# Kernel tuning notes

Hardware: AMD Instinct MI355X
Metric: run time of the kernel (lower is better)

The kernel has to match this reference:

```python
import jax, jax.numpy as jnp
import numpy as np

BETA = 0.02  # soft-argmax temperature (CATs / matchsplat default)


def _resize_bilinear_ac(x, out_h, out_w):
    """Bilinear resize over the last two dims, align_corners=True (matches F.interpolate)."""
    H, W = x.shape[-2], x.shape[-1]
    ys = jnp.linspace(0.0, H - 1.0, out_h)
    xs = jnp.linspace(0.0, W - 1.0, out_w)
    y0 = jnp.floor(ys).astype(jnp.int32)
    y1 = jnp.minimum(y0 + 1, H - 1)
    x0 = jnp.floor(xs).astype(jnp.int32)
    x1 = jnp.minimum(x0 + 1, W - 1)
    wy = (ys - y0).astype(x.dtype)
    wx = (xs - x0).astype(x.dtype)
    rows = x[..., y0, :] * (1.0 - wy)[:, None] + x[..., y1, :] * wy[:, None]
    return rows[..., x0] * (1.0 - wx) + rows[..., x1] * wx


def _correlation(f0, f1):
    # f0, f1: [B, C, H, W] -> dense 4D cost volume [B, H0, W0, H1, W1], scaled by 1/sqrt(C)
    b, c, h, w = f0.shape
    return jnp.einsum('bchw,bcuv->bhwuv', f0, f1) / (c ** 0.5)


def _interpolate4d(x, size):
    # x: [B, ch, h1, w1, h2, w2]; separable bilinear over (h2,w2) then (h1,w1), align_corners=True
    B, ch, h1, w1, h2, w2 = x.shape
    x = _resize_bilinear_ac(x.reshape(B, ch * h1 * w1, h2, w2), size[2], size[3])
    x = x.reshape(B, ch, h1, w1, size[2], size[3])
    x = jnp.transpose(x, (0, 1, 4, 5, 2, 3)).reshape(B, ch * size[2] * size[3], h1, w1)
    x = _resize_bilinear_ac(x, size[0], size[1])
    x = x.reshape(B, ch, size[2], size[3], size[0], size[1])
    return jnp.transpose(x, (0, 1, 4, 5, 2, 3))


def _soft_argmax(corr):
    # corr: [B, Hs*Ws, Ht, Wt]; softmax over source positions per target pixel,
    # then marginal expectations of normalized [-1,1] coordinates.
    b, c, h, w = corr.shape
    prob = jax.nn.softmax(corr / BETA, axis=1).reshape(b, h, w, h, w)
    x_normal = jnp.linspace(-1.0, 1.0, w, dtype=corr.dtype)
    y_normal = jnp.linspace(-1.0, 1.0, h, dtype=corr.dtype)
    grid_x = (prob.sum(axis=1) * x_normal[None, :, None, None]).sum(axis=1)[:, None]  # [B,1,h,w]
    grid_y = (prob.sum(axis=2) * y_normal[None, :, None, None]).sum(axis=1)[:, None]
    return grid_x, grid_y


def _mapping_to_flow(mapping):
    # mapping: [B,2,H,W] normalized coords in [-1,1] -> pixel-space flow (map - identity grid)
    B, _, H, W = mapping.shape
    mx = (mapping[:, 0] + 1.0) * (W - 1) / 2.0
    my = (mapping[:, 1] + 1.0) * (H - 1) / 2.0
    gx = jnp.arange(W, dtype=mapping.dtype)[None, :]
    gy = jnp.arange(H, dtype=mapping.dtype)[:, None]
    return jnp.stack([mx - gx, my - gy], axis=1)


def _forward(feat0_c, feat1_c, feat0_f, feat1_f):
    B = feat0_c.shape[0]
    S = 64
    corr_c = _correlation(feat0_c, feat1_c)                        # [B,32,32,32,32]
    corr_c = _interpolate4d(corr_c[:, None], (S, S, S, S))[:, 0]   # [B,64,64,64,64]
    corr_f = _correlation(feat0_f, feat1_f)                        # [B,64,64,64,64]
    c = ((corr_c + corr_f) * 0.5)[:, None]                         # [B,1,64,64,64,64]
    c_flip = jnp.transpose(c, (0, 1, 4, 5, 2, 3))
    gx, gy = _soft_argmax(c_flip.reshape(B, S * S, S, S))
    flow = _mapping_to_flow(jnp.concatenate([gx, gy], axis=1))
    gxf, gyf = _soft_argmax(c.reshape(B, S * S, S, S))
    flow_flip = _mapping_to_flow(jnp.concatenate([gxf, gyf], axis=1))
    trans_features = jnp.stack([feat0_f, feat1_f], axis=1)         # [B,2,C,64,64]
    tc = jnp.stack([feat0_c, feat1_c], axis=1)
    C = tc.shape[2]
    tc = _resize_bilinear_ac(tc.reshape(B * 2, C, tc.shape[-2], tc.shape[-1]), S, S)
    trans_features_coarse = tc.reshape(B, 2, C, S, S)
    return trans_features, trans_features_coarse, c, c_flip, flow, flow_flip


def setup_inputs():
    key = jax.random.key(0)
    k0, k1, k2, k3 = jax.random.split(key, 4)
    B, C = 2, 128
    return {
        'feat0_c': jax.random.normal(k0, (B, C, 32, 32), dtype=jnp.float32),
        'feat1_c': jax.random.normal(k1, (B, C, 32, 32), dtype=jnp.float32),
        'feat0_f': jax.random.normal(k2, (B, C, 64, 64), dtype=jnp.float32),
        'feat1_f': jax.random.normal(k3, (B, C, 64, 64), dtype=jnp.float32),
    }


def reference(feat0_c, feat1_c, feat0_f, feat1_f):
    return _forward(feat0_c, feat1_c, feat0_f, feat1_f)
```

## Files before the change

### kernel.cpp

```cpp
#include <hip/hip_runtime.h>
#include <math.h>

#define SCALE_C 0.08838834764831845f
#define INV_BETA 50.0f
#define STEP63 (2.0f / 63.0f)

typedef short bf16x8 __attribute__((ext_vector_type(8)));
typedef float f32x4 __attribute__((ext_vector_type(4)));

__device__ __forceinline__ void interp_coef32(int t, int& i0, int& i1, float& w) {
    float s = (float)(t * 31) / 63.0f;
    i0 = (int)floorf(s);
    if (i0 > 31) i0 = 31;
    i1 = i0 + 1;
    if (i1 > 31) i1 = 31;
    w = s - (float)i0;
}

__global__ __launch_bounds__(256) void k_corr_c(const float* __restrict__ f0c,
                                                const float* __restrict__ f1c,
                                                float* __restrict__ ws) {
    __shared__ float As[16][64];
    __shared__ float Bs[16][64];
    const int b = blockIdx.z;
    const int m0 = blockIdx.y * 64, n0 = blockIdx.x * 64;
    const float* A  = f0c + (long long)b * 131072;
    const float* Bp = f1c + (long long)b * 131072;
    const int tid = threadIdx.x;
    const int tx = tid & 15, ty = tid >> 4;
    const int lk = tid >> 4;
    const int lc = (tid & 15) * 4;
    float acc[4][4] = {{0.f}};
    for (int k0 = 0; k0 < 128; k0 += 16) {
        *(float4*)&As[lk][lc] = *(const float4*)&A[(k0 + lk) * 1024 + m0 + lc];
        *(float4*)&Bs[lk][lc] = *(const float4*)&Bp[(k0 + lk) * 1024 + n0 + lc];
        __syncthreads();
#pragma unroll
        for (int kk = 0; kk < 16; ++kk) {
            float4 a4 = *(float4*)&As[kk][ty * 4];
            float4 b4 = *(float4*)&Bs[kk][tx * 4];
            float av[4] = {a4.x, a4.y, a4.z, a4.w};
            float bv[4] = {b4.x, b4.y, b4.z, b4.w};
#pragma unroll
            for (int i = 0; i < 4; ++i)
#pragma unroll
                for (int j = 0; j < 4; ++j)
                    acc[i][j] = fmaf(av[i], bv[j], acc[i][j]);
        }
        __syncthreads();
    }
#pragma unroll
    for (int i = 0; i < 4; ++i) {
        float4 w4 = make_float4(acc[i][0] * SCALE_C, acc[i][1] * SCALE_C,
                                acc[i][2] * SCALE_C, acc[i][3] * SCALE_C);
        *(float4*)&ws[(long long)b * 1048576 + (long long)(m0 + ty * 4 + i) * 1024 + n0 + tx * 4] = w4;
    }
}

__global__ __launch_bounds__(256) void k_split(const float* __restrict__ f0f,
                                               const float* __restrict__ f1f,
                                               unsigned short* __restrict__ hi,
                                               unsigned short* __restrict__ lo) {
    __shared__ unsigned int t[64 * 132];
    const int m = blockIdx.y;
    const int pt = blockIdx.x;
    const float* src = ((m >> 1) ? f1f : f0f) + (size_t)(m & 1) * 524288 + pt * 64;
    const int tid = threadIdx.x;
#pragma unroll
    for (int p = 0; p < 8; ++p) {
        int k = p * 16 + (tid >> 4);
        int px = (tid & 15) * 4;
        float4 v = *(const float4*)&src[(size_t)k * 4096 + px];
        float vv[4] = {v.x, v.y, v.z, v.w};
#pragma unroll
        for (int j = 0; j < 4; ++j) {
            float x = vv[j];
            unsigned int u = __float_as_uint(x);
            unsigned int h = (u + 0x7FFFu + ((u >> 16) & 1u)) >> 16;
            float r = x - __uint_as_float(h << 16);
            unsigned int ur = __float_as_uint(r);
            unsigned int l2 = (ur + 0x7FFFu + ((ur >> 16) & 1u)) >> 16;
            t[(px + j) * 132 + k] = h | (l2 << 16);
        }
    }
    __syncthreads();
    const int row = tid >> 2, ks = (tid & 3) * 32;
    size_t obase = ((size_t)m * 4096 + (size_t)pt * 64 + row) * 128 + ks;
#pragma unroll
    for (int c = 0; c < 4; ++c) {
        unsigned int u[8];
        *(uint4*)&u[0] = *(const uint4*)&t[row * 132 + ks + c * 8];
        *(uint4*)&u[4] = *(const uint4*)&t[row * 132 + ks + c * 8 + 4];
        uint4 ho, lw;
        ho.x = (u[0] & 0xFFFFu) | (u[1] << 16);
        ho.y = (u[2] & 0xFFFFu) | (u[3] << 16);
        ho.z = (u[4] & 0xFFFFu) | (u[5] << 16);
        ho.w = (u[6] & 0xFFFFu) | (u[7] << 16);
        lw.x = (u[0] >> 16) | (u[1] & 0xFFFF0000u);
        lw.y = (u[2] >> 16) | (u[3] & 0xFFFF0000u);
        lw.z = (u[4] >> 16) | (u[5] & 0xFFFF0000u);
        lw.w = (u[6] >> 16) | (u[7] & 0xFFFF0000u);
        *(uint4*)&hi[obase + c * 8] = ho;
        *(uint4*)&lo[obase + c * 8] = lw;
    }
}

__global__ __launch_bounds__(256, 3) void k_fused2(const unsigned short* __restrict__ planes,
                                                   const float* __restrict__ cws,
                                                   float* __restrict__ c_out,
                                                   float* __restrict__ cf_out,
                                                   float* __restrict__ parts) {
    __shared__ __attribute__((aligned(16))) float smem[8448];
    const int b = blockIdx.z, by = blockIdx.y, bx = blockIdx.x;
    const int tid = threadIdx.x;
    const int wv = tid >> 6, lane = tid & 63;
    const int lr = lane & 15, lq = lane >> 4;
    const int wr = wv >> 1, wc = wv & 1;

    {
        const float* Cc = cws + (size_t)b * 1048576;
        for (int e = tid; e < 8192; e += 256) {
            int pair = e >> 11, rem = e & 2047;
            int xc0 = rem >> 6, x1 = rem & 63;
            int s0 = pair >> 1, s1 = pair & 1;
            int ya, yb; float wy0; interp_coef32(2 * by + s0, ya, yb, wy0);
            int za, zb; float wy1; interp_coef32(2 * bx + s1, za, zb, wy1);
            int xa, xb; float wx1; interp_coef32(x1, xa, xb, wx1);
            const float* r0 = Cc + (size_t)(ya * 32 + xc0) * 1024;
            const float* r1 = Cc + (size_t)(yb * 32 + xc0) * 1024;
            float g0 = (r0[za * 32 + xa] * (1.f - wy1) + r0[zb * 32 + xa] * wy1) * (1.f - wy0)
                     + (r1[za * 32 + xa] * (1.f - wy1) + r1[zb * 32 + xa] * wy1) * wy0;
            float g1 = (r0[za * 32 + xb] * (1.f - wy1) + r0[zb * 32 + xb] * wy1) * (1.f - wy0)
                     + (r1[za * 32 + xb] * (1.f - wy1) + r1[zb * 32 + xb] * wy1) * wy0;
            smem[(pair * 64 + x1) * 33 + xc0] = g0 * (1.f - wx1) + g1 * wx1;
        }
    }

    const unsigned short* Ah = planes + (size_t)b * 524288       + (size_t)(by * 128 + wr * 64) * 128;
    const unsigned short* Bh = planes + (size_t)(2 + b) * 524288 + (size_t)(bx * 128 + wc * 64) * 128;
    f32x4 acc[4][4];
#pragma unroll
    for (int i = 0; i < 4; ++i)
#pragma unroll
        for (int j = 0; j < 4; ++j) acc[i][j] = (f32x4){0.f, 0.f, 0.f, 0.f};

#pragma unroll 2
    for (int kc = 0; kc < 4; ++kc) {
        const int ko = kc * 32 + lq * 8;
        bf16x8 ah[4], al[4], bh[4], bl[4];
#pragma unroll
        for (int t = 0; t < 4; ++t) {
            const unsigned short* pa = Ah + (size_t)(t * 16 + lr) * 128 + ko;
            const unsigned short* pb = Bh + (size_t)(t * 16 + lr) * 128 + ko;
            ah[t] = *(const bf16x8*)pa;
            al[t] = *(const bf16x8*)(pa + 2097152);
            bh[t] = *(const bf16x8*)pb;
            bl[t] = *(const bf16x8*)(pb + 2097152);
        }
#pragma unroll
        for (int ni = 0; ni < 4; ++ni)
#pragma unroll
            for (int mi = 0; mi < 4; ++mi) {
                f32x4 a = acc[mi][ni];
                a = __builtin_amdgcn_mfma_f32_16x16x32_bf16(ah[mi], bh[ni], a, 0, 0, 0);
                a = __builtin_amdgcn_mfma_f32_16x16x32_bf16(al[mi], bh[ni], a, 0, 0, 0);
                a = __builtin_amdgcn_mfma_f32_16x16x32_bf16(ah[mi], bl[ni], a, 0, 0, 0);
                acc[mi][ni] = a;
            }
    }

    __syncthreads();

#pragma unroll
    for (int mi = 0; mi < 4; ++mi)
#pragma unroll
        for (int dr = 0; dr < 4; ++dr) {
            int x0 = mi * 16 + lq * 4 + dr;
            float s = (float)(x0 * 31) / 63.0f;
            int i0 = (int)s;
            float w = s - (float)i0;
            int i1 = i0 + 1; if (i1 > 31) i1 = 31;
#pragma unroll
            for (int ni = 0; ni < 4; ++ni) {
                const float* t2 = &smem[(wv * 64 + ni * 16 + lr) * 33];
                float up = t2[i0] * (1.f - w) + t2[i1] * w;
                acc[mi][ni][dr] = (acc[mi][ni][dr] * SCALE_C + up) * 0.5f;
            }
        }

    const int rowbase = by * 128 + wr * 64, colbase = bx * 128 + wc * 64;
    {
        size_t fb = ((size_t)b << 24) + (size_t)colbase * 4096 + rowbase;
#pragma unroll
        for (int mi = 0; mi < 4; ++mi)
#pragma unroll
            for (int ni = 0; ni < 4; ++ni) {
                int co = ni * 16 + lr;
                *(float4*)&cf_out[fb + (size_t)co * 4096 + mi * 16 + lq * 4] =
                    make_float4(acc[mi][ni][0], acc[mi][ni][1], acc[mi][ni][2], acc[mi][ni][3]);
            }
    }

#pragma unroll
    for (int r = 0; r < 2; ++r) {
        __syncthreads();
        if (wr == r) {
#pragma unroll
            for (int mi = 0; mi < 4; ++mi)
#pragma unroll
                for (int dr = 0; dr < 4; ++dr) {
                    int rl = mi * 16 + lq * 4 + dr;
                    int sw = (rl & 7) << 2;
#pragma unroll
                    for (int ni = 0; ni < 4; ++ni) {
                        int col = wc * 64 + ni * 16 + lr;
                        int c4 = col >> 2;
                        smem[rl * 132 + ((c4 ^ sw) << 2) + (col & 3)] = acc[mi][ni][dr];
                    }
                }
        }
        __syncthreads();
        size_t cb = ((size_t)b << 24) + (size_t)(by * 128 + r * 64) * 4096 + bx * 128;
#pragma unroll
        for (int i = 0; i < 8; ++i) {
            int f = tid + i * 256;
            int rl = f >> 5, c4 = f & 31;
            float4 v = *(float4*)&smem[rl * 132 + ((c4 ^ ((rl & 7) << 2)) << 2)];
            *(float4*)&c_out[cb + (size_t)rl * 4096 + c4 * 4] = v;
        }
    }

    float4* pred4 = (float4*)smem;
    float4* parts4 = (float4*)parts;
    __syncthreads();

    {
        float yn1 = -1.f + (float)(2 * bx + wc) * STEP63;
#pragma unroll
        for (int mi = 0; mi < 4; ++mi)
#pragma unroll
            for (int dr = 0; dr < 4; ++dr) {
                float m = fmaxf(fmaxf(acc[mi][0][dr], acc[mi][1][dr]),
                                fmaxf(acc[mi][2][dr], acc[mi][3][dr]));
                m = fmaxf(m, __shfl_xor(m, 1, 64));
                m = fmaxf(m, __shfl_xor(m, 2, 64));
                m = fmaxf(m, __shfl_xor(m, 4, 64));
                m = fmaxf(m, __shfl_xor(m, 8, 64));
                float l = 0.f, sx = 0.f;
#pragma unroll
                for (int ni = 0; ni < 4; ++ni) {
                    float e = __expf((acc[mi][ni][dr] - m) * INV_BETA);
                    l += e;
                    sx += e * (-1.f + (float)(ni * 16 + lr) * STEP63);
                }
                l += __shfl_xor(l, 1, 64);  sx += __shfl_xor(sx, 1, 64);
                l += __shfl_xor(l, 2, 64);  sx += __shfl_xor(sx, 2, 64);
                l += __shfl_xor(l, 4, 64);  sx += __shfl_xor(sx, 4, 64);
                l += __shfl_xor(l, 8, 64);  sx += __shfl_xor(sx, 8, 64);
                if (lr == 0)
                    pred4[wc * 128 + wr * 64 + mi * 16 + lq * 4 + dr] = make_float4(m, l, sx, yn1 * l);
            }
    }
    __syncthreads();
    if (tid < 128) {
        float4 h0 = pred4[tid], h1 = pred4[128 + tid];
        float M = fmaxf(h0.x, h1.x);
        float s0 = __expf((h0.x - M) * INV_BETA);
        float s1 = __expf((h1.x - M) * INV_BETA);
        parts4[((size_t)b * 4096 + by * 128 + tid) * 32 + bx] =
            make_float4(M, h0.y * s0 + h1.y * s1, h0.z * s0 + h1.z * s1, h0.w * s0 + h1.w * s1);
    }
    __syncthreads();

    {
        float yn0 = -1.f + (float)(2 * by + wr) * STEP63;
#pragma unroll
        for (int ni = 0; ni < 4; ++ni) {
            float m = acc[0][ni][0];
#pragma unroll
            for (int mi = 0; mi < 4; ++mi)
#pragma unroll
                for (int dr = 0; dr < 4; ++dr) m = fmaxf(m, acc[mi][ni][dr]);
            m = fmaxf(m, __shfl_xor(m, 16, 64));
            m = fmaxf(m, __shfl_xor(m, 32, 64));
            float l = 0.f, sx = 0.f;
#pragma unroll
            for (int mi = 0; mi < 4; ++mi)
#pragma unroll
                for (int dr = 0; dr < 4; ++dr) {
                    float e = __expf((acc[mi][ni][dr] - m) * INV_BETA);
                    l += e;
                    sx += e * (-1.f + (float)(mi * 16 + lq * 4 + dr) * STEP63);
                }
            l += __shfl_xor(l, 16, 64);  sx += __shfl_xor(sx, 16, 64);
            l += __shfl_xor(l, 32, 64);  sx += __shfl_xor(sx, 32, 64);
            if (lq == 0)
                pred4[wr * 128 + wc * 64 + ni * 16 + lr] = make_float4(m, l, sx, yn0 * l);
        }
    }
    __syncthreads();
    if (tid < 128) {
        float4 h0 = pred4[tid], h1 = pred4[128 + tid];
        float M = fmaxf(h0.x, h1.x);
        float s0 = __expf((h0.x - M) * INV_BETA);
        float s1 = __expf((h1.x - M) * INV_BETA);
        parts4[262144 + ((size_t)b * 4096 + bx * 128 + tid) * 32 + by] =
            make_float4(M, h0.y * s0 + h1.y * s1, h0.z * s0 + h1.z * s1, h0.w * s0 + h1.w * s1);
    }
}

__global__ __launch_bounds__(256) void k_flow(const float* __restrict__ parts,
                                              float* __restrict__ flow,
                                              float* __restrict__ flowf) {
    const int row = blockIdx.x * 4 + (threadIdx.x >> 6);
    const int lane = threadIdx.x & 63;
    const float4* p4 = (const float4*)parts + (long long)row * 32;
    float m = -1e30f, l = 0.f, sx = 0.f, sy = 0.f;
    if (lane < 32) { float4 v = p4[lane]; m = v.x; l = v.y; sx = v.z; sy = v.w; }
    float M = m;
#pragma unroll
    for (int off = 1; off < 64; off <<= 1) M = fmaxf(M, __shfl_xor(M, off, 64));
    float s = __expf((m - M) * INV_BETA);
    l *= s; sx *= s; sy *= s;
#pragma unroll
    for (int off = 1; off < 64; off <<= 1) {
        l += __shfl_xor(l, off, 64);
        sx += __shfl_xor(sx, off, 64);
        sy += __shfl_xor(sy, off, 64);
    }
    if (lane == 0) {
        float gx = sx / l, gy = sy / l;
        float mx = (gx + 1.f) * 31.5f, my = (gy + 1.f) * 31.5f;
        int dir = row >> 13, b = (row >> 12) & 1, p = row & 4095;
        float* o = dir ? flowf : flow;
        o[(long long)b * 8192 + p] = mx - (float)(p & 63);
        o[(long long)b * 8192 + 4096 + p] = my - (float)(p >> 6);
    }
}

__global__ void k_copy_trans(const float* __restrict__ f0f, const float* __restrict__ f1f,
                             float* __restrict__ out1) {
    int idx = blockIdx.x * 256 + threadIdx.x;
    int bv = idx >> 17;
    int r = idx & 131071;
    int b = bv >> 1, v = bv & 1;
    const float4* src = (const float4*)(v ? f1f : f0f) + (long long)b * 131072 + r;
    ((float4*)out1)[idx] = *src;
}

__global__ void k_coarse(const float* __restrict__ f0c, const float* __restrict__ f1c,
                         float* __restrict__ out2) {
    int idx = blockIdx.x * 256 + threadIdx.x;
    int x = idx & 63, y = (idx >> 6) & 63, ch = (idx >> 12) & 127;
    int v = (idx >> 19) & 1, b = idx >> 20;
    int iy0, iy1; float wy; interp_coef32(y, iy0, iy1, wy);
    int ix0, ix1; float wx; interp_coef32(x, ix0, ix1, wx);
    const float* src = (v ? f1c : f0c) + (long long)(b * 128 + ch) * 1024;
    float a  = src[iy0 * 32 + ix0] * (1.f - wy) + src[iy1 * 32 + ix0] * wy;
    float c2 = src[iy0 * 32 + ix1] * (1.f - wy) + src[iy1 * 32 + ix1] * wy;
    out2[idx] = a * (1.f - wx) + c2 * wx;
}

__global__ __launch_bounds__(256) void k_fused_fb(const float* __restrict__ f0f,
                                                  const float* __restrict__ f1f,
                                                  const float* __restrict__ cws,
                                                  float* __restrict__ c_out,
                                                  float* __restrict__ cf_out) {
    __shared__ float As[16][64];
    __shared__ float Bs[16][64];
    __shared__ float tmp[32][33];
    const int b = blockIdx.z, y0 = blockIdx.y, y1 = blockIdx.x;
    const int tid = threadIdx.x;
    const int tx = tid & 15, ty = tid >> 4;
    const float* A  = f0f + (long long)b * 524288 + y0 * 64;
    const float* Bp = f1f + (long long)b * 524288 + y1 * 64;
    int iy0a, iy0b; float wy0; interp_coef32(y0, iy0a, iy0b, wy0);
    int iy1a, iy1b; float wy1; interp_coef32(y1, iy1a, iy1b, wy1);
    const float* Cc = cws + (long long)b * 1048576;
    for (int r = tid; r < 1024; r += 256) {
        int i = r >> 5, j = r & 31;
        const float* ra = Cc + (long long)(iy0a * 32 + i) * 1024;
        const float* rb = Cc + (long long)(iy0b * 32 + i) * 1024;
        float va = ra[iy1a * 32 + j] * (1.f - wy1) + ra[iy1b * 32 + j] * wy1;
        float vb = rb[iy1a * 32 + j] * (1.f - wy1) + rb[iy1b * 32 + j] * wy1;
        tmp[i][j] = va * (1.f - wy0) + vb * wy0;
    }
    float acc[4][4] = {{0.f}};
    const int lk = tid >> 4;
    const int lc = (tid & 15) * 4;
    for (int k0 = 0; k0 < 128; k0 += 16) {
        *(float4*)&As[lk][lc] = *(const float4*)&A[(long long)(k0 + lk) * 4096 + lc];
        *(float4*)&Bs[lk][lc] = *(const float4*)&Bp[(long long)(k0 + lk) * 4096 + lc];
        __syncthreads();
#pragma unroll
        for (int kk = 0; kk < 16; ++kk) {
            float4 a4 = *(float4*)&As[kk][ty * 4];
            float4 b4 = *(float4*)&Bs[kk][tx * 4];
            float av[4] = {a4.x, a4.y, a4.z, a4.w};
            float bv[4] = {b4.x, b4.y, b4.z, b4.w};
#pragma unroll
            for (int i = 0; i < 4; ++i)
#pragma unroll
                for (int j = 0; j < 4; ++j)
                    acc[i][j] = fmaf(av[i], bv[j], acc[i][j]);
        }
        __syncthreads();
    }
    int ix0a[4], ix0b[4]; float wx0[4];
    int ix1a[4], ix1b[4]; float wx1[4];
#pragma unroll
    for (int i = 0; i < 4; ++i) interp_coef32(ty * 4 + i, ix0a[i], ix0b[i], wx0[i]);
#pragma unroll
    for (int j = 0; j < 4; ++j) interp_coef32(tx * 4 + j, ix1a[j], ix1b[j], wx1[j]);
    float val[4][4];
#pragma unroll
    for (int i = 0; i < 4; ++i)
#pragma unroll
        for (int j = 0; j < 4; ++j) {
            float ta = tmp[ix0a[i]][ix1a[j]] * (1.f - wx1[j]) + tmp[ix0a[i]][ix1b[j]] * wx1[j];
            float tb = tmp[ix0b[i]][ix1a[j]] * (1.f - wx1[j]) + tmp[ix0b[i]][ix1b[j]] * wx1[j];
            val[i][j] = (acc[i][j] * SCALE_C + (ta * (1.f - wx0[i]) + tb * wx0[i])) * 0.5f;
        }
    const long long cbase = ((long long)b << 24) + (long long)(y0 * 64) * 4096 + y1 * 64;
#pragma unroll
    for (int i = 0; i < 4; ++i)
        *(float4*)&c_out[cbase + (long long)(ty * 4 + i) * 4096 + tx * 4] =
            make_float4(val[i][0], val[i][1], val[i][2], val[i][3]);
    const long long fbase = ((long long)b << 24) + (long long)(y1 * 64) * 4096 + y0 * 64;
#pragma unroll
    for (int j = 0; j < 4; ++j)
        *(float4*)&cf_out[fbase + (long long)(tx * 4 + j) * 4096 + ty * 4] =
            make_float4(val[0][j], val[1][j], val[2][j], val[3][j]);
}

__global__ __launch_bounds__(256) void k_softargmax(const float* __restrict__ cmat,
                                                    float* __restrict__ flow_out) {
    const int tid = threadIdx.x;
    const float4* src = (const float4*)cmat + (long long)blockIdx.x * 1024;
    float4 r0 = src[tid];
    float4 r1 = src[tid + 256];
    float4 r2 = src[tid + 512];
    float4 r3 = src[tid + 768];
    float m = fmaxf(fmaxf(fmaxf(r0.x, r0.y), fmaxf(r0.z, r0.w)),
                    fmaxf(fmaxf(r1.x, r1.y), fmaxf(r1.z, r1.w)));
    m = fmaxf(m, fmaxf(fmaxf(r2.x, r2.y), fmaxf(r2.z, r2.w)));
    m = fmaxf(m, fmaxf(fmaxf(r3.x, r3.y), fmaxf(r3.z, r3.w)));
    __shared__ float red[16];
    const int lane = tid & 63, wave = tid >> 6;
#pragma unroll
    for (int off = 32; off > 0; off >>= 1) m = fmaxf(m, __shfl_xor(m, off, 64));
    if (lane == 0) red[wave] = m;
    __syncthreads();
    m = fmaxf(fmaxf(red[0], red[1]), fmaxf(red[2], red[3]));
    float l = 0.f, sx = 0.f, sy = 0.f;
#pragma unroll
    for (int s = 0; s < 4; ++s) {
        float4 r = (s == 0) ? r0 : (s == 1) ? r1 : (s == 2) ? r2 : r3;
        int f = tid + s * 256;
        float yn = -1.f + (float)(f >> 4) * STEP63;
        float xb = (float)((f & 15) * 4);
        float e0 = __expf((r.x - m) * 50.f);
        float e1 = __expf((r.y - m) * 50.f);
        float e2 = __expf((r.z - m) * 50.f);
        float e3 = __expf((r.w - m) * 50.f);
        float es = e0 + e1 + e2 + e3;
        l += es;
        sy += es * yn;
        sx += e0 * (-1.f + xb * STEP63) + e1 * (-1.f + (xb + 1.f) * STEP63)
            + e2 * (-1.f + (xb + 2.f) * STEP63) + e3 * (-1.f + (xb + 3.f) * STEP63);
    }
#pragma unroll
    for (int off = 32; off > 0; off >>= 1) {
        l  += __shfl_xor(l, off, 64);
        sx += __shfl_xor(sx, off, 64);
        sy += __shfl_xor(sy, off, 64);
    }
    if (lane == 0) { red[4 + wave] = l; red[8 + wave] = sx; red[12 + wave] = sy; }
    __syncthreads();
    if (tid == 0) {
        float L  = red[4] + red[5] + red[6] + red[7];
        float SX = red[8] + red[9] + red[10] + red[11];
        float SY = red[12] + red[13] + red[14] + red[15];
        float mx = (SX / L + 1.f) * 31.5f;
        float my = (SY / L + 1.f) * 31.5f;
        int bi = blockIdx.x;
        int b = bi >> 12, p = bi & 4095;
        flow_out[(long long)b * 8192 + p]        = mx - (float)(p & 63);
        flow_out[(long long)b * 8192 + 4096 + p] = my - (float)(p >> 6);
    }
}

extern "C" void kernel_launch(void* const* d_in, const int* in_sizes, int n_in,
                              void* d_out, int out_size, void* d_ws, size_t ws_size,
                              hipStream_t stream) {
    const float* f0c = (const float*)d_in[0];
    const float* f1c = (const float*)d_in[1];
    const float* f0f = (const float*)d_in[2];
    const float* f1f = (const float*)d_in[3];
    float* out = (float*)d_out;

    float* c_out  = out + 4194304;
    float* cf_out = out + 37748736;
    float* flow   = out + 71303168;
    float* flowf  = out + 71319552;

    if (ws_size >= (size_t)16777216) {
        float* parts = (float*)d_ws;
        float* cws   = parts + 2097152;
        unsigned short* hi = (unsigned short*)out;
        unsigned short* lo = hi + 2097152;
        k_split<<<dim3(64, 4, 1), 256, 0, stream>>>(f0f, f1f, hi, lo);
        k_corr_c<<<dim3(16, 16, 2), 256, 0, stream>>>(f0c, f1c, cws);
        k_fused2<<<dim3(32, 32, 2), 256, 0, stream>>>(hi, cws, c_out, cf_out, parts);
        k_flow<<<4096, 256, 0, stream>>>(parts, flow, flowf);
        k_copy_trans<<<2048, 256, 0, stream>>>(f0f, f1f, out);
        k_coarse<<<8192, 256, 0, stream>>>(f0c, f1c, out + 2097152);
    } else {
        float* corr_ws = out;
        k_corr_c<<<dim3(16, 16, 2), 256, 0, stream>>>(f0c, f1c, corr_ws);
        k_fused_fb<<<dim3(64, 64, 2), 256, 0, stream>>>(f0f, f1f, corr_ws, c_out, cf_out);
        k_copy_trans<<<2048, 256, 0, stream>>>(f0f, f1f, out);
        k_coarse<<<8192, 256, 0, stream>>>(f0c, f1c, out + 2097152);
        k_softargmax<<<8192, 256, 0, stream>>>(c_out, flow);
        k_softargmax<<<8192, 256, 0, stream>>>(cf_out, flowf);
    }
}
```

Baseline: 424.6 us.

## Stage coarse-volume patch in LDS and coalesce transposed cost-volume stores

The coarse correlation upsampling prologue now loads a small 3x32x3x32 patch of the coarse volume into shared memory once, then does separable bilinear interpolation in two LDS passes. Previously it gathered eight scattered global values per output element. The transposed c_flip output is also staged through a swizzled shared-memory tile, so it is written with fully coalesced float4 rows instead of strided per-lane float4 stores. The cost is a larger LDS footprint (13440 floats) and extra barriers, which may reduce occupancy below the requested three blocks per CU.

```diff
diff --git a/kernel.cpp b/kernel.cpp
--- a/kernel.cpp
+++ b/kernel.cpp
@@ -110,29 +110,56 @@
                                                    float* __restrict__ c_out,
                                                    float* __restrict__ cf_out,
                                                    float* __restrict__ parts) {
-    __shared__ __attribute__((aligned(16))) float smem[8448];
+    __shared__ __attribute__((aligned(16))) float smem[13440];
+    float* const Freg = smem + 9216;
     const int b = blockIdx.z, by = blockIdx.y, bx = blockIdx.x;
     const int tid = threadIdx.x;
     const int wv = tid >> 6, lane = tid & 63;
     const int lr = lane & 15, lq = lane >> 4;
     const int wr = wv >> 1, wc = wv & 1;
 
+    const int y0base = (2 * by * 31) / 63;
+    const int y1base = (2 * bx * 31) / 63;
+
     {
         const float* Cc = cws + (size_t)b * 1048576;
-        for (int e = tid; e < 8192; e += 256) {
-            int pair = e >> 11, rem = e & 2047;
-            int xc0 = rem >> 6, x1 = rem & 63;
-            int s0 = pair >> 1, s1 = pair & 1;
+        for (int e = tid; e < 9216; e += 256) {
+            int x1c = e & 31;
+            int q = e >> 5;
+            int r = (q * 21846) >> 16;
+            int dy1 = q - r * 3;
+            int x0c = r & 31;
+            int dy0 = r >> 5;
+            int y0r = y0base + dy0; if (y0r > 31) y0r = 31;
+            int y1r = y1base + dy1; if (y1r > 31) y1r = 31;
+            smem[e] = Cc[(size_t)(y0r * 32 + x0c) * 1024 + y1r * 32 + x1c];
+        }
+    }
+    __syncthreads();
+
+    {
+        for (int e = tid; e < 4096; e += 256) {
+            int x1c = e & 31, x0c = (e >> 5) & 31, p = e >> 10;
+            int s0 = p >> 1, s1 = p & 1;
             int ya, yb; float wy0; interp_coef32(2 * by + s0, ya, yb, wy0);
             int za, zb; float wy1; interp_coef32(2 * bx + s1, za, zb, wy1);
+            int a0 = ya - y0base, a1 = yb - y0base;
+            int b0 = za - y1base, b1 = zb - y1base;
+            const float* s00 = &smem[((a0 * 32 + x0c) * 3) * 32 + x1c];
+            const float* s10 = &smem[((a1 * 32 + x0c) * 3) * 32 + x1c];
+            float g0 = s00[b0 * 32] * (1.f - wy1) + s00[b1 * 32] * wy1;
+            float g1 = s10[b0 * 32] * (1.f - wy1) + s10[b1 * 32] * wy1;
+            Freg[(p * 32 + x0c) * 33 + x1c] = g0 * (1.f - wy0) + g1 * wy0;
+        }
+    }
+    __syncthreads();
+
+    {
+        for (int e = tid; e < 8192; e += 256) {
+            int x1 = e & 63, x0c = (e >> 6) & 31, p = e >> 11;
             int xa, xb; float wx1; interp_coef32(x1, xa, xb, wx1);
-            const float* r0 = Cc + (size_t)(ya * 32 + xc0) * 1024;
-            const float* r1 = Cc + (size_t)(yb * 32 + xc0) * 1024;
-            float g0 = (r0[za * 32 + xa] * (1.f - wy1) + r0[zb * 32 + xa] * wy1) * (1.f - wy0)
-                     + (r1[za * 32 + xa] * (1.f - wy1) + r1[zb * 32 + xa] * wy1) * wy0;
-            float g1 = (r0[za * 32 + xb] * (1.f - wy1) + r0[zb * 32 + xb] * wy1) * (1.f - wy0)
-                     + (r1[za * 32 + xb] * (1.f - wy1) + r1[zb * 32 + xb] * wy1) * wy0;
-            smem[(pair * 64 + x1) * 33 + xc0] = g0 * (1.f - wx1) + g1 * wx1;
+            const float* Fp = &Freg[(p * 32 + x0c) * 33];
+            smem[(p * 64 + x1) * 33 + x0c] = Fp[xa] * (1.f - wx1) + Fp[xb] * wx1;
         }
     }
 
@@ -188,19 +215,6 @@
             }
         }
 
-    const int rowbase = by * 128 + wr * 64, colbase = bx * 128 + wc * 64;
-    {
-        size_t fb = ((size_t)b << 24) + (size_t)colbase * 4096 + rowbase;
-#pragma unroll
-        for (int mi = 0; mi < 4; ++mi)
-#pragma unroll
-            for (int ni = 0; ni < 4; ++ni) {
-                int co = ni * 16 + lr;
-                *(float4*)&cf_out[fb + (size_t)co * 4096 + mi * 16 + lq * 4] =
-                    make_float4(acc[mi][ni][0], acc[mi][ni][1], acc[mi][ni][2], acc[mi][ni][3]);
-            }
-    }
-
 #pragma unroll
     for (int r = 0; r < 2; ++r) {
         __syncthreads();
@@ -227,6 +241,33 @@
             int rl = f >> 5, c4 = f & 31;
             float4 v = *(float4*)&smem[rl * 132 + ((c4 ^ ((rl & 7) << 2)) << 2)];
             *(float4*)&c_out[cb + (size_t)rl * 4096 + c4 * 4] = v;
+        }
+    }
+
+#pragma unroll
+    for (int r = 0; r < 2; ++r) {
+        __syncthreads();
+        if (wc == r) {
+#pragma unroll
+            for (int ni = 0; ni < 4; ++ni) {
+                int col = ni * 16 + lr;
+                int sw = (col & 7) << 2;
+#pragma unroll
+                for (int mi = 0; mi < 4; ++mi) {
+                    int q = wr * 16 + mi * 4 + lq;
+                    *(float4*)&smem[col * 132 + ((q ^ sw) << 2)] =
+                        make_float4(acc[mi][ni][0], acc[mi][ni][1], acc[mi][ni][2], acc[mi][ni][3]);
+                }
+            }
+        }
+        __syncthreads();
+        size_t fb = ((size_t)b << 24) + (size_t)(bx * 128 + r * 64) * 4096 + by * 128;
+#pragma unroll
+        for (int i = 0; i < 8; ++i) {
+            int f = tid + i * 256;
+            int col = f >> 5, q = f & 31;
+            float4 v = *(float4*)&smem[col * 132 + ((q ^ ((col & 7) << 2)) << 2)];
+            *(float4*)&cf_out[fb + (size_t)col * 4096 + q * 4] = v;
         }
     }
 
```

Result: faster. 408.3 us (-3.8%).
